# Kernel optimization log

Measured on AMD Instinct MI355X. Metric: run time of the kernel, lower is better.

The kernel has to match this reference:

```python
import jax, jax.numpy as jnp
import numpy as np

B, L, D = 8, 2048, 64


def setup_inputs() -> dict:
    key = jax.random.key(0)
    kq, kk, kv = jax.random.split(key, 3)
    query = jax.random.normal(kq, (B, L, D), dtype=jnp.float32)
    key_t = jax.random.normal(kk, (B, L, D), dtype=jnp.float32)
    value = jax.random.normal(kv, (B, L, D), dtype=jnp.float32)
    return {"query": query, "key": key_t, "value": value}


def reference(query, key, value):
    d = query.shape[-1]
    # e = Q K^T / sqrt(d_k)   -> [B, Lq, Lk]
    scale = 1.0 / np.sqrt(float(d)).astype(np.float32)
    e = jnp.einsum("bqd,bkd->bqk", query, key) * scale
    # stable softmax over keys (matches exp(e - max)/sum in source)
    attention = jax.nn.softmax(e, axis=-1)
    # v = A V   -> [B, Lq, Dv]
    return jnp.einsum("bqk,bkd->bqd", attention, value)
```

## Files before the change

kernel.cpp:

```cpp
#include <hip/hip_runtime.h>


#define B_ 8
#define L_ 2048
#define D_ 64
#define NT 256
#define PS 40
#define TK 32
#define NTILE 16

typedef _Float16 half8_t __attribute__((ext_vector_type(8)));
typedef float f32x4 __attribute__((ext_vector_type(4)));

#define SCALE_LOG2E 0.1803368801111244f

__global__ __launch_bounds__(NT) void prepass(
    const float* __restrict__ K, const float* __restrict__ V,
    _Float16* __restrict__ K16, _Float16* __restrict__ VT16)
{
    const int blk = blockIdx.x;
    const int t = threadIdx.x;
    if (blk < 512) {
        const int i = blk * NT + t;
        const float4* s4 = (const float4*)K;
        const float4 a = s4[2 * i], b = s4[2 * i + 1];
        half8_t w;
        w[0] = (_Float16)a.x; w[1] = (_Float16)a.y;
        w[2] = (_Float16)a.z; w[3] = (_Float16)a.w;
        w[4] = (_Float16)b.x; w[5] = (_Float16)b.y;
        w[6] = (_Float16)b.z; w[7] = (_Float16)b.w;
        ((half8_t*)K16)[i] = w;
    } else {
        __shared__ __align__(16) _Float16 Lt[64 * 72];
        const int vblk = blk - 512;
        const int bb = vblk >> 5;
        const int kt = vblk & 31;
        const int r  = t >> 2;
        const int ch = t & 3;
        const float* vrow = V + ((size_t)bb * L_ + kt * 64 + r) * D_ + ch * 16;
        #pragma unroll
        for (int i = 0; i < 4; ++i) {
            const float4 f = ((const float4*)vrow)[i];
            const int d0 = ch * 16 + i * 4;
            Lt[(d0 + 0) * 72 + r] = (_Float16)f.x;
            Lt[(d0 + 1) * 72 + r] = (_Float16)f.y;
            Lt[(d0 + 2) * 72 + r] = (_Float16)f.z;
            Lt[(d0 + 3) * 72 + r] = (_Float16)f.w;
        }
        __syncthreads();
        const int d  = t >> 2;
        const int c2 = t & 3;
        const half8_t w0 = *(const half8_t*)&Lt[d * 72 + c2 * 16];
        const half8_t w1 = *(const half8_t*)&Lt[d * 72 + c2 * 16 + 8];
        _Float16* orow = VT16 + ((size_t)bb * D_ + d) * L_ + kt * 64 + c2 * 16;
        *(half8_t*)orow = w0;
        *(half8_t*)(orow + 8) = w1;
    }
}


#define STAGE(TP, PW, PR, BKC, BKN, BVP, DO_PF)                                 \
    {                                                                           \
        const int kb_pf = key0 + ((TP) + 1) * TK;                               \
        if (DO_PF) {                                                            \
            _Pragma("unroll") for (int s = 0; s < 2; ++s)                       \
            _Pragma("unroll") for (int c = 0; c < 2; ++c)                       \
                BKN[s][c] = *(const half8_t*)&Kb[(size_t)(kb_pf + s * 16 + l15) * D_ + c * 32 + quad * 8]; \
        }                                                                       \
        f32x4 sc[2][2];                                                         \
        _Pragma("unroll") for (int qs = 0; qs < 2; ++qs)                        \
        _Pragma("unroll") for (int s = 0; s < 2; ++s) {                         \
            f32x4 acc = (f32x4){0.f, 0.f, 0.f, 0.f};                            \
            acc = __builtin_amdgcn_mfma_f32_16x16x32_f16(aq[qs][0], BKC[s][0], acc, 0, 0, 0); \
            acc = __builtin_amdgcn_mfma_f32_16x16x32_f16(aq[qs][1], BKC[s][1], acc, 0, 0, 0); \
            sc[qs][s] = acc;                                                    \
        }                                                                       \
        _Pragma("unroll") for (int qs = 0; qs < 2; ++qs)                        \
        _Pragma("unroll") for (int s = 0; s < 2; ++s)                           \
        _Pragma("unroll") for (int r = 0; r < 4; ++r) {                         \
            const float p = __builtin_exp2f(sc[qs][s][r]);                      \
            lacc[qs][r] += p;                                                   \
            PW[(qs * 16 + quad * 4 + r) * PS + s * 16 + l15] = (_Float16)p;     \
        }                                                                       \
        half8_t ap[2];                                                          \
        _Pragma("unroll") for (int qs = 0; qs < 2; ++qs)                        \
            ap[qs] = *(const half8_t*)&PR[(qs * 16 + l15) * PS + quad * 8];     \
        _Pragma("unroll") for (int qs = 0; qs < 2; ++qs)                        \
        _Pragma("unroll") for (int d = 0; d < 4; ++d)                           \
            ofr[qs][d] = __builtin_amdgcn_mfma_f32_16x16x32_f16(ap[qs], BVP[d], ofr[qs][d], 0, 0, 0); \
        if (DO_PF) {                                                            \
            _Pragma("unroll") for (int d = 0; d < 4; ++d)                       \
                BVP[d] = *(const half8_t*)&Vb[(size_t)(d * 16 + l15) * L_ + kb_pf + quad * 8]; \
        }                                                                       \
    }

__global__ __launch_bounds__(NT) void attn_sw(
    const float* __restrict__ Q,
    const _Float16* __restrict__ K16,
    const _Float16* __restrict__ VT16,
    float* __restrict__ O)
{
    __shared__ __align__(16) _Float16 P0s[4][32 * PS];
    __shared__ __align__(16) _Float16 P1s[4][32 * PS];
    __shared__ float Ored[256 * 33];
    __shared__ float Lred[128];

    const int t    = threadIdx.x;
    const int wave = t >> 6;
    const int lane = t & 63;
    const int quad = lane >> 4;
    const int l15  = lane & 15;

    const int b   = blockIdx.x & 7;
    const int qbi = blockIdx.x >> 3;
    const int qb  = qbi * 32;
    const int key0 = wave * (TK * NTILE);

    _Float16* P0w = P0s[wave];
    _Float16* P1w = P1s[wave];

    const _Float16* Kb = K16 + (size_t)b * L_ * D_;
    const _Float16* Vb = VT16 + (size_t)b * D_ * L_;

    half8_t aq[2][2];
    #pragma unroll
    for (int qs = 0; qs < 2; ++qs) {
        const float* qp = Q + ((size_t)b * L_ + qb + qs * 16 + l15) * D_ + quad * 8;
        #pragma unroll
        for (int c = 0; c < 2; ++c) {
            const float4 f0 = *(const float4*)(qp + c * 32);
            const float4 f1 = *(const float4*)(qp + c * 32 + 4);
            aq[qs][c][0] = (_Float16)(f0.x * SCALE_LOG2E);
            aq[qs][c][1] = (_Float16)(f0.y * SCALE_LOG2E);
            aq[qs][c][2] = (_Float16)(f0.z * SCALE_LOG2E);
            aq[qs][c][3] = (_Float16)(f0.w * SCALE_LOG2E);
            aq[qs][c][4] = (_Float16)(f1.x * SCALE_LOG2E);
            aq[qs][c][5] = (_Float16)(f1.y * SCALE_LOG2E);
            aq[qs][c][6] = (_Float16)(f1.z * SCALE_LOG2E);
            aq[qs][c][7] = (_Float16)(f1.w * SCALE_LOG2E);
        }
    }

    f32x4 ofr[2][4];
    #pragma unroll
    for (int qs = 0; qs < 2; ++qs)
        #pragma unroll
        for (int d = 0; d < 4; ++d)
            ofr[qs][d] = (f32x4){0.f, 0.f, 0.f, 0.f};
    float lacc[2][4] = {{0.f, 0.f, 0.f, 0.f}, {0.f, 0.f, 0.f, 0.f}};

    half8_t bk0[2][2], bk1[2][2], bv0[4], bv1[4];
    #pragma unroll
    for (int s = 0; s < 2; ++s)
        #pragma unroll
        for (int c = 0; c < 2; ++c) {
            bk0[s][c] = *(const half8_t*)&Kb[(size_t)(key0 + s * 16 + l15) * D_ + c * 32 + quad * 8];
            bk1[s][c] = *(const half8_t*)&Kb[(size_t)(key0 + TK + s * 16 + l15) * D_ + c * 32 + quad * 8];
        }
    #pragma unroll
    for (int d = 0; d < 4; ++d) {
        bv0[d] = *(const half8_t*)&Vb[(size_t)(d * 16 + l15) * L_ + key0 + quad * 8];
        bv1[d] = *(const half8_t*)&Vb[(size_t)(d * 16 + l15) * L_ + key0 + TK + quad * 8];
    }
    {
        f32x4 sc[2][2];
        #pragma unroll
        for (int qs = 0; qs < 2; ++qs)
            #pragma unroll
            for (int s = 0; s < 2; ++s) {
                f32x4 acc = (f32x4){0.f, 0.f, 0.f, 0.f};
                acc = __builtin_amdgcn_mfma_f32_16x16x32_f16(aq[qs][0], bk0[s][0], acc, 0, 0, 0);
                acc = __builtin_amdgcn_mfma_f32_16x16x32_f16(aq[qs][1], bk0[s][1], acc, 0, 0, 0);
                sc[qs][s] = acc;
            }
        #pragma unroll
        for (int qs = 0; qs < 2; ++qs)
            #pragma unroll
            for (int s = 0; s < 2; ++s)
                #pragma unroll
                for (int r = 0; r < 4; ++r) {
                    const float p = __builtin_exp2f(sc[qs][s][r]);
                    lacc[qs][r] += p;
                    P0w[(qs * 16 + quad * 4 + r) * PS + s * 16 + l15] = (_Float16)p;
                }
    }

    for (int tp = 1; tp <= 13; tp += 2) {
        STAGE(tp,     P1w, P0w, bk1, bk0, bv0, true)
        STAGE(tp + 1, P0w, P1w, bk0, bk1, bv1, true)
    }
    STAGE(15, P1w, P0w, bk1, bk0, bv0, false)

    {
        half8_t ap[2];
        #pragma unroll
        for (int qs = 0; qs < 2; ++qs)
            ap[qs] = *(const half8_t*)&P1w[(qs * 16 + l15) * PS + quad * 8];
        #pragma unroll
        for (int qs = 0; qs < 2; ++qs)
            #pragma unroll
            for (int d = 0; d < 4; ++d)
                ofr[qs][d] = __builtin_amdgcn_mfma_f32_16x16x32_f16(ap[qs], bv1[d], ofr[qs][d], 0, 0, 0);
    }

    #pragma unroll
    for (int qs = 0; qs < 2; ++qs)
        #pragma unroll
        for (int r = 0; r < 4; ++r) {
            float v = lacc[qs][r];
            v += __shfl_xor(v, 1, 64);
            v += __shfl_xor(v, 2, 64);
            v += __shfl_xor(v, 4, 64);
            v += __shfl_xor(v, 8, 64);
            lacc[qs][r] = v;
        }

    #pragma unroll
    for (int qs = 0; qs < 2; ++qs)
        #pragma unroll
        for (int d = 0; d < 4; ++d)
            #pragma unroll
            for (int r = 0; r < 4; ++r)
                Ored[(wave * 64 + lane) * 33 + qs * 16 + d * 4 + r] = ofr[qs][d][r];
    if (l15 == 0) {
        #pragma unroll
        for (int qs = 0; qs < 2; ++qs)
            #pragma unroll
            for (int r = 0; r < 4; ++r)
                Lred[wave * 32 + qs * 16 + quad * 4 + r] = lacc[qs][r];
    }
    __syncthreads();

    #pragma unroll
    for (int qs = 0; qs < 2; ++qs)
        #pragma unroll
        for (int r = 0; r < 4; ++r) {
            float osum = 0.f;
            #pragma unroll
            for (int w2 = 0; w2 < 4; ++w2)
                osum += Ored[(w2 * 64 + lane) * 33 + qs * 16 + wave * 4 + r];
            const int row = qs * 16 + quad * 4 + r;
            const float lt = Lred[row] + Lred[32 + row] + Lred[64 + row] + Lred[96 + row];
            O[((size_t)b * L_ + qb + row) * D_ + wave * 16 + l15] = osum / lt;
        }
}

#define KS 72
__global__ __launch_bounds__(NT) void attn_mfma_f16(
    const float* __restrict__ Q, const float* __restrict__ K,
    const float* __restrict__ V, float* __restrict__ O)
{
    __shared__ __align__(16) _Float16 Kt[64 * KS];
    __shared__ __align__(16) _Float16 Vt[D_ * KS];
    __shared__ __align__(16) _Float16 Pt[4][16 * KS];

    const int t = threadIdx.x;
    const int wave = t >> 6, lane = t & 63, quad = lane >> 4, l15 = lane & 15;
    const int bpb = L_ / 64;
    const int b = blockIdx.x / bpb;
    const int qb = (blockIdx.x % bpb) * 64 + wave * 16;
    const size_t boff = (size_t)b * L_ * D_;

    half8_t aq[2];
    {
        const float* qp = Q + boff + (size_t)(qb + l15) * D_ + quad * 8;
        #pragma unroll
        for (int c = 0; c < 2; ++c) {
            const float4* p4 = (const float4*)(qp + c * 32);
            const float4 f0 = p4[0], f1 = p4[1];
            aq[c][0] = (_Float16)f0.x; aq[c][1] = (_Float16)f0.y;
            aq[c][2] = (_Float16)f0.z; aq[c][3] = (_Float16)f0.w;
            aq[c][4] = (_Float16)f1.x; aq[c][5] = (_Float16)f1.y;
            aq[c][6] = (_Float16)f1.z; aq[c][7] = (_Float16)f1.w;
        }
    }
    f32x4 ofr[4];
    #pragma unroll
    for (int d = 0; d < 4; ++d) ofr[d] = (f32x4){0.f, 0.f, 0.f, 0.f};
    float lacc[4] = {0.f, 0.f, 0.f, 0.f};
    const int skey = t & 63, sdg = t >> 6;
    _Float16* Pw = &Pt[wave][0];

    for (int kt = 0; kt < L_ / 64; ++kt) {
        __syncthreads();
        {
            const float4* kg4 = (const float4*)(K + boff + (size_t)(kt * 64 + skey) * D_ + sdg * 16);
            const float4 f0 = kg4[0], f1 = kg4[1], f2 = kg4[2], f3 = kg4[3];
            half8_t w0, w1;
            w0[0] = (_Float16)f0.x; w0[1] = (_Float16)f0.y;
            w0[2] = (_Float16)f0.z; w0[3] = (_Float16)f0.w;
            w0[4] = (_Float16)f1.x; w0[5] = (_Float16)f1.y;
            w0[6] = (_Float16)f1.z; w0[7] = (_Float16)f1.w;
            w1[0] = (_Float16)f2.x; w1[1] = (_Float16)f2.y;
            w1[2] = (_Float16)f2.z; w1[3] = (_Float16)f2.w;
            w1[4] = (_Float16)f3.x; w1[5] = (_Float16)f3.y;
            w1[6] = (_Float16)f3.z; w1[7] = (_Float16)f3.w;
            *(half8_t*)&Kt[skey * KS + sdg * 16] = w0;
            *(half8_t*)&Kt[skey * KS + sdg * 16 + 8] = w1;
        }
        {
            const float4* vg4 = (const float4*)(V + boff + (size_t)(kt * 64 + skey) * D_ + sdg * 16);
            #pragma unroll
            for (int i = 0; i < 4; ++i) {
                const float4 f = vg4[i];
                const int d0 = sdg * 16 + i * 4;
                Vt[(d0 + 0) * KS + skey] = (_Float16)f.x;
                Vt[(d0 + 1) * KS + skey] = (_Float16)f.y;
                Vt[(d0 + 2) * KS + skey] = (_Float16)f.z;
                Vt[(d0 + 3) * KS + skey] = (_Float16)f.w;
            }
        }
        __syncthreads();
        #pragma unroll
        for (int s = 0; s < 4; ++s) {
            const half8_t bk0 = *(const half8_t*)&Kt[(s * 16 + l15) * KS + quad * 8];
            const half8_t bk1 = *(const half8_t*)&Kt[(s * 16 + l15) * KS + 32 + quad * 8];
            f32x4 sc = (f32x4){0.f, 0.f, 0.f, 0.f};
            sc = __builtin_amdgcn_mfma_f32_16x16x32_f16(aq[0], bk0, sc, 0, 0, 0);
            sc = __builtin_amdgcn_mfma_f32_16x16x32_f16(aq[1], bk1, sc, 0, 0, 0);
            #pragma unroll
            for (int r = 0; r < 4; ++r) {
                const float p = __expf(sc[r] * 0.125f);
                lacc[r] += p;
                Pw[(quad * 4 + r) * KS + s * 16 + l15] = (_Float16)p;
            }
        }
        __syncthreads();
        #pragma unroll
        for (int c = 0; c < 2; ++c) {
            const half8_t ap = *(const half8_t*)&Pw[l15 * KS + c * 32 + quad * 8];
            #pragma unroll
            for (int d = 0; d < 4; ++d) {
                const half8_t bv = *(const half8_t*)&Vt[(d * 16 + l15) * KS + c * 32 + quad * 8];
                ofr[d] = __builtin_amdgcn_mfma_f32_16x16x32_f16(ap, bv, ofr[d], 0, 0, 0);
            }
        }
    }
    #pragma unroll
    for (int r = 0; r < 4; ++r) {
        float v = lacc[r];
        v += __shfl_xor(v, 1, 64);
        v += __shfl_xor(v, 2, 64);
        v += __shfl_xor(v, 4, 64);
        v += __shfl_xor(v, 8, 64);
        lacc[r] = v;
    }
    #pragma unroll
    for (int r = 0; r < 4; ++r) {
        const float inv = 1.0f / lacc[r];
        float* orow = O + boff + (size_t)(qb + quad * 4 + r) * D_ + l15;
        #pragma unroll
        for (int d = 0; d < 4; ++d) orow[d * 16] = ofr[d][r] * inv;
    }
}

extern "C" void kernel_launch(void* const* d_in, const int* in_sizes, int n_in,
                              void* d_out, int out_size, void* d_ws, size_t ws_size,
                              hipStream_t stream) {
    const float* Q = (const float*)d_in[0];
    const float* K = (const float*)d_in[1];
    const float* V = (const float*)d_in[2];
    float* O = (float*)d_out;

    if (ws_size >= (size_t)8 * 1024 * 1024) {
        _Float16* K16  = (_Float16*)d_ws;
        _Float16* VT16 = K16 + (size_t)B_ * L_ * D_;
        prepass<<<768, NT, 0, stream>>>(K, V, K16, VT16);
        attn_sw<<<512, NT, 0, stream>>>(Q, K16, VT16, O);
    } else {
        attn_mfma_f16<<<256, NT, 0, stream>>>(Q, K, V, O);
    }
}
```

Measured before the change: 98.35 us.

## Compute transposed scores so P stays in registers via shuffles, no LDS

Swaps the MFMA operand order so the score tile comes out as S^T, with keys along rows. The exp'd probabilities are packed to fp16 pairs and redistributed across lanes with __shfl into the A-operand layout for the PV MFMA. This removes the per-wave LDS P buffers and their write/read round trip. The row-sum accumulation now reduces across quads instead of across the 16 lanes. Prefetching is restructured into a simple A/B register double buffer. The cost is extra cross-lane shuffle and select instructions, plus a different prefetch schedule.

```diff
diff --git a/kernel.cpp b/kernel.cpp
--- a/kernel.cpp
+++ b/kernel.cpp
@@ -5,11 +5,11 @@
 #define L_ 2048
 #define D_ 64
 #define NT 256
-#define PS 40
 #define TK 32
-#define NTILE 16
 
 typedef _Float16 half8_t __attribute__((ext_vector_type(8)));
+typedef _Float16 half2v __attribute__((ext_vector_type(2)));
+typedef int int4v __attribute__((ext_vector_type(4)));
 typedef float f32x4 __attribute__((ext_vector_type(4)));
 
 #define SCALE_LOG2E 0.1803368801111244f
@@ -59,49 +59,65 @@
 }
 
 
-#define STAGE(TP, PW, PR, BKC, BKN, BVP, DO_PF)                                 \
+#define LOADT(KB, BK, BV)                                                       \
     {                                                                           \
-        const int kb_pf = key0 + ((TP) + 1) * TK;                               \
-        if (DO_PF) {                                                            \
-            _Pragma("unroll") for (int s = 0; s < 2; ++s)                       \
-            _Pragma("unroll") for (int c = 0; c < 2; ++c)                       \
-                BKN[s][c] = *(const half8_t*)&Kb[(size_t)(kb_pf + s * 16 + l15) * D_ + c * 32 + quad * 8]; \
+        _Pragma("unroll") for (int s = 0; s < 2; ++s)                           \
+        _Pragma("unroll") for (int c = 0; c < 2; ++c)                           \
+            BK[s][c] = *(const half8_t*)&Kb[(size_t)((KB) + s * 16 + l15) * D_ + c * 32 + quad * 8]; \
+        _Pragma("unroll") for (int d = 0; d < 4; ++d)                           \
+            BV[d] = *(const half8_t*)&Vb[(size_t)(d * 16 + l15) * L_ + (KB) + quad * 8]; \
+    }
+
+#define PROC(BK, BV)                                                            \
+    {                                                                           \
+        f32x4 sc[2][2];                                                         \
+        _Pragma("unroll") for (int ks = 0; ks < 2; ++ks)                        \
+        _Pragma("unroll") for (int qs = 0; qs < 2; ++qs) {                      \
+            f32x4 acc = (f32x4){0.f, 0.f, 0.f, 0.f};                            \
+            acc = __builtin_amdgcn_mfma_f32_16x16x32_f16(BK[ks][0], bq[qs][0], acc, 0, 0, 0); \
+            acc = __builtin_amdgcn_mfma_f32_16x16x32_f16(BK[ks][1], bq[qs][1], acc, 0, 0, 0); \
+            sc[ks][qs] = acc;                                                   \
         }                                                                       \
-        f32x4 sc[2][2];                                                         \
-        _Pragma("unroll") for (int qs = 0; qs < 2; ++qs)                        \
-        _Pragma("unroll") for (int s = 0; s < 2; ++s) {                         \
-            f32x4 acc = (f32x4){0.f, 0.f, 0.f, 0.f};                            \
-            acc = __builtin_amdgcn_mfma_f32_16x16x32_f16(aq[qs][0], BKC[s][0], acc, 0, 0, 0); \
-            acc = __builtin_amdgcn_mfma_f32_16x16x32_f16(aq[qs][1], BKC[s][1], acc, 0, 0, 0); \
-            sc[qs][s] = acc;                                                    \
+        int pk[2][2][2];                                                        \
+        _Pragma("unroll") for (int ks = 0; ks < 2; ++ks)                        \
+        _Pragma("unroll") for (int qs = 0; qs < 2; ++qs) {                      \
+            const float p0 = __builtin_exp2f(sc[ks][qs][0]);                    \
+            const float p1 = __builtin_exp2f(sc[ks][qs][1]);                    \
+            const float p2 = __builtin_exp2f(sc[ks][qs][2]);                    \
+            const float p3 = __builtin_exp2f(sc[ks][qs][3]);                    \
+            lacc[qs] += (p0 + p1) + (p2 + p3);                                  \
+            half2v h01; h01[0] = (_Float16)p0; h01[1] = (_Float16)p1;           \
+            half2v h23; h23[0] = (_Float16)p2; h23[1] = (_Float16)p3;           \
+            pk[ks][qs][0] = __builtin_bit_cast(int, h01);                       \
+            pk[ks][qs][1] = __builtin_bit_cast(int, h23);                       \
         }                                                                       \
-        _Pragma("unroll") for (int qs = 0; qs < 2; ++qs)                        \
-        _Pragma("unroll") for (int s = 0; s < 2; ++s)                           \
-        _Pragma("unroll") for (int r = 0; r < 4; ++r) {                         \
-            const float p = __builtin_exp2f(sc[qs][s][r]);                      \
-            lacc[qs][r] += p;                                                   \
-            PW[(qs * 16 + quad * 4 + r) * PS + s * 16 + l15] = (_Float16)p;     \
+        _Pragma("unroll") for (int qs = 0; qs < 2; ++qs) {                      \
+            const int srcA = ((quad & 1) << 5) + l15;                           \
+            const int srcB = srcA + 16;                                         \
+            const int a0 = __shfl(pk[0][qs][0], srcA, 64);                      \
+            const int b0 = __shfl(pk[1][qs][0], srcA, 64);                      \
+            const int a1 = __shfl(pk[0][qs][1], srcA, 64);                      \
+            const int b1 = __shfl(pk[1][qs][1], srcA, 64);                      \
+            const int a2 = __shfl(pk[0][qs][0], srcB, 64);                      \
+            const int b2 = __shfl(pk[1][qs][0], srcB, 64);                      \
+            const int a3 = __shfl(pk[0][qs][1], srcB, 64);                      \
+            const int b3 = __shfl(pk[1][qs][1], srcB, 64);                      \
+            const bool hi = quad >= 2;                                          \
+            int4v dw;                                                           \
+            dw[0] = hi ? b0 : a0; dw[1] = hi ? b1 : a1;                         \
+            dw[2] = hi ? b2 : a2; dw[3] = hi ? b3 : a3;                         \
+            const half8_t ap = __builtin_bit_cast(half8_t, dw);                 \
+            _Pragma("unroll") for (int d = 0; d < 4; ++d)                       \
+                ofr[qs][d] = __builtin_amdgcn_mfma_f32_16x16x32_f16(ap, BV[d], ofr[qs][d], 0, 0, 0); \
         }                                                                       \
-        half8_t ap[2];                                                          \
-        _Pragma("unroll") for (int qs = 0; qs < 2; ++qs)                        \
-            ap[qs] = *(const half8_t*)&PR[(qs * 16 + l15) * PS + quad * 8];     \
-        _Pragma("unroll") for (int qs = 0; qs < 2; ++qs)                        \
-        _Pragma("unroll") for (int d = 0; d < 4; ++d)                           \
-            ofr[qs][d] = __builtin_amdgcn_mfma_f32_16x16x32_f16(ap[qs], BVP[d], ofr[qs][d], 0, 0, 0); \
-        if (DO_PF) {                                                            \
-            _Pragma("unroll") for (int d = 0; d < 4; ++d)                       \
-                BVP[d] = *(const half8_t*)&Vb[(size_t)(d * 16 + l15) * L_ + kb_pf + quad * 8]; \
-        }                                                                       \
-    }
-
-__global__ __launch_bounds__(NT) void attn_sw(
+    }
+
+__global__ __launch_bounds__(NT) void attn_bp(
     const float* __restrict__ Q,
     const _Float16* __restrict__ K16,
     const _Float16* __restrict__ VT16,
     float* __restrict__ O)
 {
-    __shared__ __align__(16) _Float16 P0s[4][32 * PS];
-    __shared__ __align__(16) _Float16 P1s[4][32 * PS];
     __shared__ float Ored[256 * 33];
     __shared__ float Lred[128];
 
@@ -114,15 +130,12 @@
     const int b   = blockIdx.x & 7;
     const int qbi = blockIdx.x >> 3;
     const int qb  = qbi * 32;
-    const int key0 = wave * (TK * NTILE);
-
-    _Float16* P0w = P0s[wave];
-    _Float16* P1w = P1s[wave];
+    const int key0 = wave * (TK * 16);
 
     const _Float16* Kb = K16 + (size_t)b * L_ * D_;
     const _Float16* Vb = VT16 + (size_t)b * D_ * L_;
 
-    half8_t aq[2][2];
+    half8_t bq[2][2];
     #pragma unroll
     for (int qs = 0; qs < 2; ++qs) {
         const float* qp = Q + ((size_t)b * L_ + qb + qs * 16 + l15) * D_ + quad * 8;
@@ -130,14 +143,14 @@
         for (int c = 0; c < 2; ++c) {
             const float4 f0 = *(const float4*)(qp + c * 32);
             const float4 f1 = *(const float4*)(qp + c * 32 + 4);
-            aq[qs][c][0] = (_Float16)(f0.x * SCALE_LOG2E);
-            aq[qs][c][1] = (_Float16)(f0.y * SCALE_LOG2E);
-            aq[qs][c][2] = (_Float16)(f0.z * SCALE_LOG2E);
-            aq[qs][c][3] = (_Float16)(f0.w * SCALE_LOG2E);
-            aq[qs][c][4] = (_Float16)(f1.x * SCALE_LOG2E);
-            aq[qs][c][5] = (_Float16)(f1.y * SCALE_LOG2E);
-            aq[qs][c][6] = (_Float16)(f1.z * SCALE_LOG2E);
-            aq[qs][c][7] = (_Float16)(f1.w * SCALE_LOG2E);
+            bq[qs][c][0] = (_Float16)(f0.x * SCALE_LOG2E);
+            bq[qs][c][1] = (_Float16)(f0.y * SCALE_LOG2E);
+            bq[qs][c][2] = (_Float16)(f0.z * SCALE_LOG2E);
+            bq[qs][c][3] = (_Float16)(f0.w * SCALE_LOG2E);
+            bq[qs][c][4] = (_Float16)(f1.x * SCALE_LOG2E);
+            bq[qs][c][5] = (_Float16)(f1.y * SCALE_LOG2E);
+            bq[qs][c][6] = (_Float16)(f1.z * SCALE_LOG2E);
+            bq[qs][c][7] = (_Float16)(f1.w * SCALE_LOG2E);
         }
     }
 
@@ -147,73 +160,29 @@
         #pragma unroll
         for (int d = 0; d < 4; ++d)
             ofr[qs][d] = (f32x4){0.f, 0.f, 0.f, 0.f};
-    float lacc[2][4] = {{0.f, 0.f, 0.f, 0.f}, {0.f, 0.f, 0.f, 0.f}};
-
-    half8_t bk0[2][2], bk1[2][2], bv0[4], bv1[4];
-    #pragma unroll
-    for (int s = 0; s < 2; ++s)
-        #pragma unroll
-        for (int c = 0; c < 2; ++c) {
-            bk0[s][c] = *(const half8_t*)&Kb[(size_t)(key0 + s * 16 + l15) * D_ + c * 32 + quad * 8];
-            bk1[s][c] = *(const half8_t*)&Kb[(size_t)(key0 + TK + s * 16 + l15) * D_ + c * 32 + quad * 8];
-        }
-    #pragma unroll
-    for (int d = 0; d < 4; ++d) {
-        bv0[d] = *(const half8_t*)&Vb[(size_t)(d * 16 + l15) * L_ + key0 + quad * 8];
-        bv1[d] = *(const half8_t*)&Vb[(size_t)(d * 16 + l15) * L_ + key0 + TK + quad * 8];
-    }
-    {
-        f32x4 sc[2][2];
-        #pragma unroll
-        for (int qs = 0; qs < 2; ++qs)
-            #pragma unroll
-            for (int s = 0; s < 2; ++s) {
-                f32x4 acc = (f32x4){0.f, 0.f, 0.f, 0.f};
-                acc = __builtin_amdgcn_mfma_f32_16x16x32_f16(aq[qs][0], bk0[s][0], acc, 0, 0, 0);
-                acc = __builtin_amdgcn_mfma_f32_16x16x32_f16(aq[qs][1], bk0[s][1], acc, 0, 0, 0);
-                sc[qs][s] = acc;
-            }
-        #pragma unroll
-        for (int qs = 0; qs < 2; ++qs)
-            #pragma unroll
-            for (int s = 0; s < 2; ++s)
-                #pragma unroll
-                for (int r = 0; r < 4; ++r) {
-                    const float p = __builtin_exp2f(sc[qs][s][r]);
-                    lacc[qs][r] += p;
-                    P0w[(qs * 16 + quad * 4 + r) * PS + s * 16 + l15] = (_Float16)p;
-                }
-    }
-
-    for (int tp = 1; tp <= 13; tp += 2) {
-        STAGE(tp,     P1w, P0w, bk1, bk0, bv0, true)
-        STAGE(tp + 1, P0w, P1w, bk0, bk1, bv1, true)
-    }
-    STAGE(15, P1w, P0w, bk1, bk0, bv0, false)
-
-    {
-        half8_t ap[2];
-        #pragma unroll
-        for (int qs = 0; qs < 2; ++qs)
-            ap[qs] = *(const half8_t*)&P1w[(qs * 16 + l15) * PS + quad * 8];
-        #pragma unroll
-        for (int qs = 0; qs < 2; ++qs)
-            #pragma unroll
-            for (int d = 0; d < 4; ++d)
-                ofr[qs][d] = __builtin_amdgcn_mfma_f32_16x16x32_f16(ap[qs], bv1[d], ofr[qs][d], 0, 0, 0);
-    }
-
-    #pragma unroll
-    for (int qs = 0; qs < 2; ++qs)
-        #pragma unroll
-        for (int r = 0; r < 4; ++r) {
-            float v = lacc[qs][r];
-            v += __shfl_xor(v, 1, 64);
-            v += __shfl_xor(v, 2, 64);
-            v += __shfl_xor(v, 4, 64);
-            v += __shfl_xor(v, 8, 64);
-            lacc[qs][r] = v;
-        }
+    float lacc[2] = {0.f, 0.f};
+
+    half8_t bkA[2][2], bvA[4], bkB[2][2], bvB[4];
+    LOADT(key0, bkA, bvA);
+    for (int it = 0; it < 8; ++it) {
+        const int kb = key0 + it * 64;
+        LOADT(kb + 32, bkB, bvB);
+        PROC(bkA, bvA);
+        LOADT(kb + 64, bkA, bvA);
+        PROC(bkB, bvB);
+    }
+
+    #pragma unroll
+    for (int qs = 0; qs < 2; ++qs) {
+        float v = lacc[qs];
+        v += __shfl_xor(v, 16, 64);
+        v += __shfl_xor(v, 32, 64);
+        lacc[qs] = v;
+    }
+    if (quad == 0) {
+        Lred[wave * 32 + l15] = lacc[0];
+        Lred[wave * 32 + 16 + l15] = lacc[1];
+    }
 
     #pragma unroll
     for (int qs = 0; qs < 2; ++qs)
@@ -222,13 +191,6 @@
             #pragma unroll
             for (int r = 0; r < 4; ++r)
                 Ored[(wave * 64 + lane) * 33 + qs * 16 + d * 4 + r] = ofr[qs][d][r];
-    if (l15 == 0) {
-        #pragma unroll
-        for (int qs = 0; qs < 2; ++qs)
-            #pragma unroll
-            for (int r = 0; r < 4; ++r)
-                Lred[wave * 32 + qs * 16 + quad * 4 + r] = lacc[qs][r];
-    }
     __syncthreads();
 
     #pragma unroll
@@ -366,7 +328,7 @@
         _Float16* K16  = (_Float16*)d_ws;
         _Float16* VT16 = K16 + (size_t)B_ * L_ * D_;
         prepass<<<768, NT, 0, stream>>>(K, V, K16, VT16);
-        attn_sw<<<512, NT, 0, stream>>>(Q, K16, VT16, O);
+        attn_bp<<<512, NT, 0, stream>>>(Q, K16, VT16, O);
     } else {
         attn_mfma_f16<<<256, NT, 0, stream>>>(Q, K, V, O);
     }
```

Result: no change. 99.76 us (+1.4%).
